# Kernel tuning notes

Hardware: AMD Instinct MI355X
Metric: run time of the kernel (lower is better)

## Reference

```python
import math
import jax, jax.numpy as jnp
import numpy as np

B, S, D = 2, 2048, 1024
H, DK = 16, 64
NUM_BUCKETS = 32
MAX_DISTANCE = 128


def _relative_position_bucket(relative_position, num_buckets=NUM_BUCKETS, max_distance=MAX_DISTANCE):
    # bidirectional=True branch (encoder / non-causal)
    n = -relative_position
    num_buckets = num_buckets // 2
    ret = (n < 0).astype(jnp.int32) * num_buckets
    n = jnp.abs(n)
    max_exact = num_buckets // 2
    is_small = n < max_exact
    # guard log(0); masked out by is_small anyway
    n_safe = jnp.maximum(n, 1).astype(jnp.float32)
    val_if_large = max_exact + (
        jnp.log(n_safe / max_exact) / math.log(max_distance / max_exact) * (num_buckets - max_exact)
    ).astype(jnp.int32)
    val_if_large = jnp.minimum(val_if_large, num_buckets - 1)
    return ret + jnp.where(is_small, n, val_if_large)


def setup_inputs() -> dict:
    key = jax.random.key(0)
    ks = jax.random.split(key, 6)
    std_q = (D * DK) ** -0.5
    std = D ** -0.5
    return {
        "x": jax.random.normal(ks[0], (B, S, D), jnp.float32),
        "q_w": jax.random.normal(ks[1], (H * DK, D), jnp.float32) * std_q,
        "k_w": jax.random.normal(ks[2], (H * DK, D), jnp.float32) * std,
        "v_w": jax.random.normal(ks[3], (H * DK, D), jnp.float32) * std,
        "o_w": jax.random.normal(ks[4], (D, H * DK), jnp.float32) * ((H * DK) ** -0.5),
        "rel_bias": jax.random.normal(ks[5], (NUM_BUCKETS, H), jnp.float32) * std,
    }


def reference(x, q_w, k_w, v_w, o_w, rel_bias):
    b, s, _ = x.shape
    # project and split heads: [B, H, S, DK]
    def proj(w):
        return (x @ w.T).reshape(b, s, H, DK).transpose(0, 2, 1, 3)
    q, k, v = proj(q_w), proj(k_w), proj(v_w)

    # T5-style unscaled attention scores: [B, H, Sq, Sk]
    scores = jnp.einsum("bhqd,bhkd->bhqk", q, k)

    # bucketed relative-position bias
    ctx = jnp.arange(s)[:, None]
    mem = jnp.arange(s)[None, :]
    rp_bucket = _relative_position_bucket(mem - ctx)  # [S, S]
    bias = rel_bias[rp_bucket]                        # [S, S, H]
    bias = bias.transpose(2, 0, 1)[None]              # [1, H, S, S]
    scores = scores + bias

    attn = jax.nn.softmax(scores, axis=-1)
    ctx_out = jnp.einsum("bhqk,bhkd->bhqd", attn, v)
    ctx_out = ctx_out.transpose(0, 2, 1, 3).reshape(b, s, H * DK)
    return ctx_out @ o_w.T
```

## Files before the change

### kernel.cpp

```cpp
#include <hip/hip_runtime.h>
#include <stdint.h>


typedef unsigned short u16;
typedef __attribute__((ext_vector_type(8))) short short8;
typedef __attribute__((ext_vector_type(4))) float float4v;
typedef __attribute__((ext_vector_type(4))) u16 ushort4v;

typedef __attribute__((address_space(1))) void void_g;
typedef __attribute__((address_space(3))) void void_l;

#define L2E 1.4426950408889634f

__device__ __forceinline__ u16 f2b(float f) {
  union { float f; uint32_t u; } v; v.f = f;
  uint32_t r = (v.u + 0x7fffu + ((v.u >> 16) & 1u)) >> 16;
  return (u16)r;
}
__device__ __forceinline__ u16 f2b_fast(float f) {
  union { float f; uint32_t u; } v; v.f = f;
  return (u16)((v.u + 0x8000u) >> 16);
}

__global__ void cvt_all(const float* __restrict__ x,  const float* __restrict__ qw,
                        const float* __restrict__ kw, const float* __restrict__ vw,
                        const float* __restrict__ ow, const float* __restrict__ rel_bias,
                        u16* __restrict__ xb, u16* __restrict__ wqkv, u16* __restrict__ owb,
                        float* __restrict__ biasT) {
  int bi = blockIdx.x;
  if (bi >= 8192) {
    int idx = (bi - 8192) * 256 + threadIdx.x;
    int h = idx >> 12, t = idx & 4095;
    if (t > 4094) { biasT[h * 4096 + 4095] = -1.0e4f; return; }
    int d = t - 2047;
    int n = -d;
    int ret = (n < 0) ? 16 : 0;
    int na = (n < 0) ? -n : n;
    int bucket;
    if (na < 8) {
      bucket = ret + na;
    } else {
      float v = logf((float)na / 8.0f) / logf(16.0f) * 8.0f;
      int vi = 8 + (int)v;
      bucket = ret + (vi > 15 ? 15 : vi);
    }
    biasT[h * 4096 + t] = (rel_bias[bucket * 16 + h] - 8.0f) * L2E;
    return;
  }
  int i = bi * 256 + threadIdx.x;
  const float* s; u16* d; int off;
  if (i < 1048576)      { s = x;  d = xb;              off = i; }
  else if (i < 1310720) { s = qw; d = wqkv;            off = i - 1048576; }
  else if (i < 1572864) { s = kw; d = wqkv + 1048576;  off = i - 1310720; }
  else if (i < 1835008) { s = vw; d = wqkv + 2097152;  off = i - 1572864; }
  else                  { s = ow; d = owb;             off = i - 1835008; }
  float4v v = ((const float4v*)s)[off];
  ushort4v o;
  o.x = f2b(v.x); o.y = f2b(v.y); o.z = f2b(v.z); o.w = f2b(v.w);
  ((ushort4v*)d)[off] = o;
}

__global__ __launch_bounds__(256, 2)
void gemm_qkv(const u16* __restrict__ A, const u16* __restrict__ W,
              u16* __restrict__ qkb, u16* __restrict__ vTp) {
  const int K = 1024;
  __shared__ __align__(16) char SM[34816];
  u16* As = (u16*)SM;
  u16* Bs = (u16*)(SM + 16384);
  const int tid = threadIdx.x;
  const int wid = tid >> 6;
  const int lane = tid & 63;
  const int row16 = lane & 15, oct = lane >> 4;
  const int tm = blockIdx.x * 128, tn = blockIdx.y * 128;
  const int wm = (wid & 1) * 64, wn = (wid >> 1) * 64;
  const int srow = lane >> 2;
  const int sc = (lane & 3) * 8;
  float4v acc[4][4] = {};
  for (int k0 = 0; k0 < K; k0 += 64) {
    __syncthreads();
#pragma unroll
    for (int i = 0; i < 4; i++) {
      const int idx = i * 4 + wid;
      const int kk = idx & 1;
      const int rb = idx >> 1;
      const int r = rb * 16 + srow;
      const int c = kk * 32 + sc;
      __builtin_amdgcn_global_load_lds((void_g*)(A + (size_t)(tm + r) * K + k0 + c),
                                       (void_l*)(As + (kk * 128 + rb * 16) * 32), 16, 0, 0);
      __builtin_amdgcn_global_load_lds((void_g*)(W + (size_t)(tn + r) * K + k0 + c),
                                       (void_l*)(Bs + (kk * 128 + rb * 16) * 32), 16, 0, 0);
    }
    __syncthreads();
#pragma unroll
    for (int kk = 0; kk < 2; kk++) {
      short8 af[4], bfr[4];
#pragma unroll
      for (int mi = 0; mi < 4; mi++)
        af[mi] = *(const short8*)(As + (kk * 128 + wm + mi * 16 + row16) * 32 + oct * 8);
#pragma unroll
      for (int ni = 0; ni < 4; ni++)
        bfr[ni] = *(const short8*)(Bs + (kk * 128 + wn + ni * 16 + row16) * 32 + oct * 8);
#pragma unroll
      for (int mi = 0; mi < 4; mi++)
#pragma unroll
        for (int ni = 0; ni < 4; ni++)
          acc[mi][ni] = __builtin_amdgcn_mfma_f32_16x16x32_bf16(af[mi], bfr[ni], acc[mi][ni], 0, 0, 0);
    }
  }

  u16* Es = (u16*)SM;
  __syncthreads();
#pragma unroll
  for (int mi = 0; mi < 4; mi++)
#pragma unroll
    for (int ni = 0; ni < 4; ni++)
#pragma unroll
      for (int r = 0; r < 4; r++)
        Es[(wm + mi * 16 + oct * 4 + r) * 136 + wn + ni * 16 + row16] = f2b(acc[mi][ni][r]);
  __syncthreads();

  if (tn < 2048) {
#pragma unroll
    for (int it = 0; it < 8; it++) {
      int idx = it * 256 + tid;
      int row = idx >> 4, c = idx & 15;
      short8 v = *(const short8*)(Es + row * 136 + c * 8);
      *(short8*)(qkb + (size_t)(tm + row) * 2048 + tn + c * 8) = v;
    }
  } else {
    const int h0 = (tn - 2048) >> 6;
    const int b = tm >> 11;
    const int s0 = tm & 2047;
#pragma unroll
    for (int it = 0; it < 8; it++) {
      int idx = it * 256 + tid;
      int dg = idx >> 4;
      int ch = idx & 15;
      short8 o;
#pragma unroll
      for (int j = 0; j < 8; j++) {
        int sp = ch * 8 + j;
        int sl = (sp & ~31) + 16 * (sp & 1) + ((sp & 31) >> 1);
        o[j] = (short)Es[sl * 136 + dg];
      }
      const int head = h0 + (dg >> 6), d = dg & 63;
      *(short8*)(vTp + ((size_t)((b * 16 + head) * 64 + d)) * 2048 + s0 + ch * 8) = o;
    }
  }
}

__global__ __launch_bounds__(256, 2)
void gemm_out(const u16* __restrict__ A, const u16* __restrict__ W,
              float* __restrict__ C) {
  const int K = 1024, N = 1024;
  __shared__ __align__(16) char SM[34816];
  u16* As = (u16*)SM;
  u16* Bs = (u16*)(SM + 16384);
  const int tid = threadIdx.x;
  const int wid = tid >> 6;
  const int lane = tid & 63;
  const int row16 = lane & 15, oct = lane >> 4;
  const int tm = blockIdx.x * 128, tn = blockIdx.y * 128;
  const int wm = (wid & 1) * 64, wn = (wid >> 1) * 64;
  const int srow = lane >> 2;
  const int sc = (lane & 3) * 8;
  float4v acc[4][4] = {};
  for (int k0 = 0; k0 < K; k0 += 64) {
    __syncthreads();
#pragma unroll
    for (int i = 0; i < 4; i++) {
      const int idx = i * 4 + wid;
      const int kk = idx & 1;
      const int rb = idx >> 1;
      const int r = rb * 16 + srow;
      const int c = kk * 32 + sc;
      __builtin_amdgcn_global_load_lds((void_g*)(A + (size_t)(tm + r) * K + k0 + c),
                                       (void_l*)(As + (kk * 128 + rb * 16) * 32), 16, 0, 0);
      __builtin_amdgcn_global_load_lds((void_g*)(W + (size_t)(tn + r) * K + k0 + c),
                                       (void_l*)(Bs + (kk * 128 + rb * 16) * 32), 16, 0, 0);
    }
    __syncthreads();
#pragma unroll
    for (int kk = 0; kk < 2; kk++) {
      short8 af[4], bfr[4];
#pragma unroll
      for (int mi = 0; mi < 4; mi++)
        af[mi] = *(const short8*)(As + (kk * 128 + wm + mi * 16 + row16) * 32 + oct * 8);
#pragma unroll
      for (int ni = 0; ni < 4; ni++)
        bfr[ni] = *(const short8*)(Bs + (kk * 128 + wn + ni * 16 + row16) * 32 + oct * 8);
#pragma unroll
      for (int mi = 0; mi < 4; mi++)
#pragma unroll
        for (int ni = 0; ni < 4; ni++)
          acc[mi][ni] = __builtin_amdgcn_mfma_f32_16x16x32_bf16(af[mi], bfr[ni], acc[mi][ni], 0, 0, 0);
    }
  }
  float* Ef = (float*)SM;
#pragma unroll
  for (int pass = 0; pass < 2; pass++) {
    __syncthreads();
    if ((wid & 1) == pass) {
#pragma unroll
      for (int mi = 0; mi < 4; mi++)
#pragma unroll
        for (int ni = 0; ni < 4; ni++)
#pragma unroll
          for (int r = 0; r < 4; r++)
            Ef[(mi * 16 + oct * 4 + r) * 132 + wn + ni * 16 + row16] = acc[mi][ni][r];
    }
    __syncthreads();
#pragma unroll
    for (int it = 0; it < 8; it++) {
      int idx = it * 256 + tid;
      int row = idx >> 5, c = idx & 31;
      float4v v = *(const float4v*)(Ef + row * 132 + c * 4);
      *(float4v*)(C + (size_t)(tm + pass * 64 + row) * N + tn + c * 4) = v;
    }
  }
}

__global__ __launch_bounds__(256, 2)
void flash_attn(const u16* __restrict__ qkb, const u16* __restrict__ vTp,
                const float* __restrict__ biasT, u16* __restrict__ ctx) {
  const int S = 2048, LDQ = 2048;
  const int qt0 = blockIdx.x * 128;
  const int h = blockIdx.y, b = blockIdx.z;
  const int tid = threadIdx.x, wid = tid >> 6, lane = tid & 63;
  const int row16 = lane & 15, oct = lane >> 4;

  __shared__ __align__(16) float biasS[2176];
  __shared__ __align__(16) u16 Ks[2][64][40];
  __shared__ __align__(16) u16 Vts[2][64][40];
  __shared__ __align__(16) u16 Pl[4][2][16][40];

  {
    const float* bsrc = biasT + h * 4096 + (1920 - qt0);
    for (int i = tid; i < 544; i += 256)
      ((float4v*)biasS)[i] = ((const float4v*)bsrc)[i];
  }
  const float bias_neg = biasT[h * 4096];
  const float bias_pos = biasT[h * 4096 + 4094];

  const u16* qbase = qkb + ((size_t)b * S + qt0 + wid * 32) * LDQ + h * 64;
  short8 qf[2][2];
#pragma unroll
  for (int f = 0; f < 2; f++)
#pragma unroll
    for (int hd = 0; hd < 2; hd++)
      qf[f][hd] = *(const short8*)(qbase + (size_t)(f * 16 + row16) * LDQ + hd * 32 + oct * 8);

  float l_r[2][4] = {};
  float4v o_acc[2][4] = {};

  const int sr = lane >> 2, c8 = (lane & 3) * 8;
  const int srow = wid * 16 + sr;
  const u16* Kst = qkb + 1024 + ((size_t)b * S + srow) * LDQ + c8 + h * 64;
  const u16* Vst = vTp + ((size_t)(b * 16 + h) * 64 + srow) * 2048 + c8;

  short8 kreg[2], vreg[2];
#pragma unroll
  for (int hd = 0; hd < 2; hd++) kreg[hd] = *(const short8*)(Kst + hd * 32);
#pragma unroll
  for (int ks = 0; ks < 2; ks++) vreg[ks] = *(const short8*)(Vst + ks * 32);

  for (int kt = 0; kt < S; kt += 64) {
    __syncthreads();
#pragma unroll
    for (int hd = 0; hd < 2; hd++) *(short8*)&Ks[hd][srow][c8] = kreg[hd];
#pragma unroll
    for (int ks = 0; ks < 2; ks++) *(short8*)&Vts[ks][srow][c8] = vreg[ks];
    __syncthreads();

    if (kt + 64 < S) {
#pragma unroll
      for (int hd = 0; hd < 2; hd++)
        kreg[hd] = *(const short8*)(Kst + (size_t)(kt + 64) * LDQ + hd * 32);
#pragma unroll
      for (int ks = 0; ks < 2; ks++)
        vreg[ks] = *(const short8*)(Vst + (kt + 64) + ks * 32);
    }

    short8 kf[4][2];
#pragma unroll
    for (int st = 0; st < 4; st++)
#pragma unroll
      for (int hd = 0; hd < 2; hd++)
        kf[st][hd] = *(const short8*)&Ks[hd][st * 16 + row16][oct * 8];

    float4v sc[2][4];
#pragma unroll
    for (int f = 0; f < 2; f++)
#pragma unroll
      for (int st = 0; st < 4; st++) {
        float4v s = {};
        s = __builtin_amdgcn_mfma_f32_16x16x32_bf16(qf[f][0], kf[st][0], s, 0, 0, 0);
        s = __builtin_amdgcn_mfma_f32_16x16x32_bf16(qf[f][1], kf[st][1], s, 0, 0, 0);
        sc[f][st] = s;
      }

    short8 vf[2][4];
#pragma unroll
    for (int ks = 0; ks < 2; ks++)
#pragma unroll
      for (int ni = 0; ni < 4; ni++)
        vf[ks][ni] = *(const short8*)&Vts[ks][ni * 16 + row16][oct * 8];

    const int dk = kt - qt0;
    const bool far = (dk >= 256) || (dk <= -192);
    if (far) {
      const float bc = (dk > 0) ? bias_pos : bias_neg;
#pragma unroll
      for (int f = 0; f < 2; f++)
#pragma unroll
        for (int st = 0; st < 4; st++)
#pragma unroll
          for (int r = 0; r < 4; r++)
            sc[f][st][r] = __builtin_amdgcn_exp2f(__builtin_fmaf(sc[f][st][r], L2E, bc));
    } else {
#pragma unroll
      for (int f = 0; f < 2; f++) {
        const int base = kt + row16 - wid * 32 - f * 16 - oct * 4 + 127;
#pragma unroll
        for (int r = 0; r < 4; r++) {
          const int i0 = base - r;
          float b0 = biasS[i0],      b1 = biasS[i0 + 16];
          float b2 = biasS[i0 + 32], b3 = biasS[i0 + 48];
          sc[f][0][r] = __builtin_amdgcn_exp2f(__builtin_fmaf(sc[f][0][r], L2E, b0));
          sc[f][1][r] = __builtin_amdgcn_exp2f(__builtin_fmaf(sc[f][1][r], L2E, b1));
          sc[f][2][r] = __builtin_amdgcn_exp2f(__builtin_fmaf(sc[f][2][r], L2E, b2));
          sc[f][3][r] = __builtin_amdgcn_exp2f(__builtin_fmaf(sc[f][3][r], L2E, b3));
        }
      }
    }

#pragma unroll
    for (int ks = 0; ks < 2; ks++)
#pragma unroll
      for (int r = 0; r < 4; r++) {
        uint32_t pk = (uint32_t)f2b_fast(sc[0][2 * ks][r]) |
                      ((uint32_t)f2b_fast(sc[0][2 * ks + 1][r]) << 16);
        *(uint32_t*)&Pl[wid][ks][oct * 4 + r][2 * row16] = pk;
      }
#pragma unroll
    for (int f = 0; f < 2; f++) {
      if (f == 1) {
#pragma unroll
        for (int ks = 0; ks < 2; ks++)
#pragma unroll
          for (int r = 0; r < 4; r++) {
            uint32_t pk = (uint32_t)f2b_fast(sc[1][2 * ks][r]) |
                          ((uint32_t)f2b_fast(sc[1][2 * ks + 1][r]) << 16);
            *(uint32_t*)&Pl[wid][ks][oct * 4 + r][2 * row16] = pk;
          }
      }
#pragma unroll
      for (int r = 0; r < 4; r++)
        l_r[f][r] += (sc[f][0][r] + sc[f][1][r]) + (sc[f][2][r] + sc[f][3][r]);
#pragma unroll
      for (int ks = 0; ks < 2; ks++) {
        short8 pf = *(const short8*)&Pl[wid][ks][row16][oct * 8];
#pragma unroll
        for (int ni = 0; ni < 4; ni++)
          o_acc[f][ni] = __builtin_amdgcn_mfma_f32_16x16x32_bf16(pf, vf[ks][ni], o_acc[f][ni], 0, 0, 0);
      }
    }
  }

#pragma unroll
  for (int f = 0; f < 2; f++) {
#pragma unroll
    for (int r = 0; r < 4; r++) {
      float v = l_r[f][r];
      v += __shfl_xor(v, 1); v += __shfl_xor(v, 2);
      v += __shfl_xor(v, 4); v += __shfl_xor(v, 8);
      l_r[f][r] = 1.0f / v;
    }
    const size_t orow = (size_t)b * S + qt0 + wid * 32 + f * 16 + oct * 4;
#pragma unroll
    for (int ni = 0; ni < 4; ni++)
#pragma unroll
      for (int r = 0; r < 4; r++)
        ctx[(orow + r) * 1024 + h * 64 + ni * 16 + row16] = f2b_fast(o_acc[f][ni][r] * l_r[f][r]);
  }
}

extern "C" void kernel_launch(void* const* d_in, const int* in_sizes, int n_in,
                              void* d_out, int out_size, void* d_ws, size_t ws_size,
                              hipStream_t stream) {
  const float* x        = (const float*)d_in[0];
  const float* q_w      = (const float*)d_in[1];
  const float* k_w      = (const float*)d_in[2];
  const float* v_w      = (const float*)d_in[3];
  const float* o_w      = (const float*)d_in[4];
  const float* rel_bias = (const float*)d_in[5];

  char* ws = (char*)d_ws;
  u16*   xb    = (u16*)(ws);
  u16*   wqkv  = (u16*)(ws + 8388608);
  u16*   owb   = (u16*)(ws + 14680064);
  u16*   qkb   = (u16*)(ws + 16777216);
  u16*   vTp   = (u16*)(ws + 33554432);
  u16*   ctxb  = (u16*)(ws + 41943040);
  float* biasT = (float*)(ws + 50331648);

  cvt_all<<<8448, 256, 0, stream>>>(x, q_w, k_w, v_w, o_w, rel_bias,
                                    xb, wqkv, owb, biasT);

  dim3 g1(4096 / 128, 3072 / 128);
  gemm_qkv<<<g1, 256, 0, stream>>>(xb, wqkv, qkb, vTp);

  dim3 g2(2048 / 128, 16, 2);
  flash_attn<<<g2, 256, 0, stream>>>(qkb, vTp, biasT, ctxb);

  dim3 g3(4096 / 128, 1024 / 128);
  gemm_out<<<g3, 256, 0, stream>>>(ctxb, owb, (float*)d_out);
}
```

Measured before the change: 187.6 us.

## Compute transposed score tiles to feed P to MFMA from registers

Swaps the MFMA operand order so each lane holds a column of scores (keys along registers), letting the softmax probabilities be packed directly into the A-operand of the PV MFMA without an LDS round trip. The V transpose layout in the projection epilogue is permuted to match the new key ordering within each 32-key chunk. Row sums become per-lane scalars reduced across lane groups at the end, and bias indexing is adjusted. This removes the per-tile LDS writes and reads of P and the associated waits, at the cost of a more intricate key permutation that must agree exactly between kernels.

```diff
diff --git a/kernel.cpp b/kernel.cpp
--- a/kernel.cpp
+++ b/kernel.cpp
@@ -6,6 +6,7 @@
 typedef __attribute__((ext_vector_type(8))) short short8;
 typedef __attribute__((ext_vector_type(4))) float float4v;
 typedef __attribute__((ext_vector_type(4))) u16 ushort4v;
+typedef __attribute__((ext_vector_type(4))) uint32_t uint4v;
 
 typedef __attribute__((address_space(1))) void void_g;
 typedef __attribute__((address_space(3))) void void_l;
@@ -140,7 +141,7 @@
 #pragma unroll
       for (int j = 0; j < 8; j++) {
         int sp = ch * 8 + j;
-        int sl = (sp & ~31) + 16 * (sp & 1) + ((sp & 31) >> 1);
+        int sl = (sp & ~31) + (((sp >> 2) & 1) << 4) + (((sp >> 3) & 3) << 2) + (sp & 3);
         o[j] = (short)Es[sl * 136 + dg];
       }
       const int head = h0 + (dg >> 6), d = dg & 63;
@@ -232,7 +233,6 @@
   __shared__ __align__(16) float biasS[2176];
   __shared__ __align__(16) u16 Ks[2][64][40];
   __shared__ __align__(16) u16 Vts[2][64][40];
-  __shared__ __align__(16) u16 Pl[4][2][16][40];
 
   {
     const float* bsrc = biasT + h * 4096 + (1920 - qt0);
@@ -250,7 +250,7 @@
     for (int hd = 0; hd < 2; hd++)
       qf[f][hd] = *(const short8*)(qbase + (size_t)(f * 16 + row16) * LDQ + hd * 32 + oct * 8);
 
-  float l_r[2][4] = {};
+  float lsum[2] = {};
   float4v o_acc[2][4] = {};
 
   const int sr = lane >> 2, c8 = (lane & 3) * 8;
@@ -294,8 +294,8 @@
 #pragma unroll
       for (int st = 0; st < 4; st++) {
         float4v s = {};
-        s = __builtin_amdgcn_mfma_f32_16x16x32_bf16(qf[f][0], kf[st][0], s, 0, 0, 0);
-        s = __builtin_amdgcn_mfma_f32_16x16x32_bf16(qf[f][1], kf[st][1], s, 0, 0, 0);
+        s = __builtin_amdgcn_mfma_f32_16x16x32_bf16(kf[st][0], qf[f][0], s, 0, 0, 0);
+        s = __builtin_amdgcn_mfma_f32_16x16x32_bf16(kf[st][1], qf[f][1], s, 0, 0, 0);
         sc[f][st] = s;
       }
 
@@ -320,46 +320,30 @@
     } else {
 #pragma unroll
       for (int f = 0; f < 2; f++) {
-        const int base = kt + row16 - wid * 32 - f * 16 - oct * 4 + 127;
-#pragma unroll
-        for (int r = 0; r < 4; r++) {
-          const int i0 = base - r;
-          float b0 = biasS[i0],      b1 = biasS[i0 + 16];
-          float b2 = biasS[i0 + 32], b3 = biasS[i0 + 48];
-          sc[f][0][r] = __builtin_amdgcn_exp2f(__builtin_fmaf(sc[f][0][r], L2E, b0));
-          sc[f][1][r] = __builtin_amdgcn_exp2f(__builtin_fmaf(sc[f][1][r], L2E, b1));
-          sc[f][2][r] = __builtin_amdgcn_exp2f(__builtin_fmaf(sc[f][2][r], L2E, b2));
-          sc[f][3][r] = __builtin_amdgcn_exp2f(__builtin_fmaf(sc[f][3][r], L2E, b3));
-        }
+        const int basef = kt + oct * 4 - wid * 32 - f * 16 - row16 + 127;
+#pragma unroll
+        for (int st = 0; st < 4; st++)
+#pragma unroll
+          for (int r = 0; r < 4; r++)
+            sc[f][st][r] = __builtin_amdgcn_exp2f(
+                __builtin_fmaf(sc[f][st][r], L2E, biasS[basef + st * 16 + r]));
       }
     }
 
 #pragma unroll
-    for (int ks = 0; ks < 2; ks++)
-#pragma unroll
-      for (int r = 0; r < 4; r++) {
-        uint32_t pk = (uint32_t)f2b_fast(sc[0][2 * ks][r]) |
-                      ((uint32_t)f2b_fast(sc[0][2 * ks + 1][r]) << 16);
-        *(uint32_t*)&Pl[wid][ks][oct * 4 + r][2 * row16] = pk;
-      }
-#pragma unroll
     for (int f = 0; f < 2; f++) {
-      if (f == 1) {
-#pragma unroll
-        for (int ks = 0; ks < 2; ks++)
-#pragma unroll
-          for (int r = 0; r < 4; r++) {
-            uint32_t pk = (uint32_t)f2b_fast(sc[1][2 * ks][r]) |
-                          ((uint32_t)f2b_fast(sc[1][2 * ks + 1][r]) << 16);
-            *(uint32_t*)&Pl[wid][ks][oct * 4 + r][2 * row16] = pk;
-          }
-      }
-#pragma unroll
-      for (int r = 0; r < 4; r++)
-        l_r[f][r] += (sc[f][0][r] + sc[f][1][r]) + (sc[f][2][r] + sc[f][3][r]);
+      lsum[f] += ((sc[f][0][0] + sc[f][0][1]) + (sc[f][0][2] + sc[f][0][3])) +
+                 ((sc[f][1][0] + sc[f][1][1]) + (sc[f][1][2] + sc[f][1][3])) +
+                 ((sc[f][2][0] + sc[f][2][1]) + (sc[f][2][2] + sc[f][2][3])) +
+                 ((sc[f][3][0] + sc[f][3][1]) + (sc[f][3][2] + sc[f][3][3]));
 #pragma unroll
       for (int ks = 0; ks < 2; ks++) {
-        short8 pf = *(const short8*)&Pl[wid][ks][row16][oct * 8];
+        uint4v pw;
+        pw.x = (uint32_t)f2b_fast(sc[f][2 * ks][0]) | ((uint32_t)f2b_fast(sc[f][2 * ks][1]) << 16);
+        pw.y = (uint32_t)f2b_fast(sc[f][2 * ks][2]) | ((uint32_t)f2b_fast(sc[f][2 * ks][3]) << 16);
+        pw.z = (uint32_t)f2b_fast(sc[f][2 * ks + 1][0]) | ((uint32_t)f2b_fast(sc[f][2 * ks + 1][1]) << 16);
+        pw.w = (uint32_t)f2b_fast(sc[f][2 * ks + 1][2]) | ((uint32_t)f2b_fast(sc[f][2 * ks + 1][3]) << 16);
+        short8 pf = __builtin_bit_cast(short8, pw);
 #pragma unroll
         for (int ni = 0; ni < 4; ni++)
           o_acc[f][ni] = __builtin_amdgcn_mfma_f32_16x16x32_bf16(pf, vf[ks][ni], o_acc[f][ni], 0, 0, 0);
@@ -369,19 +353,19 @@
 
 #pragma unroll
   for (int f = 0; f < 2; f++) {
-#pragma unroll
-    for (int r = 0; r < 4; r++) {
-      float v = l_r[f][r];
-      v += __shfl_xor(v, 1); v += __shfl_xor(v, 2);
-      v += __shfl_xor(v, 4); v += __shfl_xor(v, 8);
-      l_r[f][r] = 1.0f / v;
-    }
+    float v = lsum[f];
+    v += __shfl_xor(v, 16);
+    v += __shfl_xor(v, 32);
+    float linv[4];
+#pragma unroll
+    for (int r = 0; r < 4; r++)
+      linv[r] = 1.0f / __shfl(v, ((lane >> 4) << 2) + r);
     const size_t orow = (size_t)b * S + qt0 + wid * 32 + f * 16 + oct * 4;
 #pragma unroll
     for (int ni = 0; ni < 4; ni++)
 #pragma unroll
       for (int r = 0; r < 4; r++)
-        ctx[(orow + r) * 1024 + h * 64 + ni * 16 + row16] = f2b_fast(o_acc[f][ni][r] * l_r[f][r]);
+        ctx[(orow + r) * 1024 + h * 64 + ni * 16 + row16] = f2b_fast(o_acc[f][ni][r] * linv[r]);
   }
 }
 
```

Measured after the change: 191.4 us. +2.0%, slower.
